# Optimization experiments

Hardware: AMD Instinct MI355X
Metric: run time of the kernel (lower is better)

Reference implementation:

```python
import jax, jax.numpy as jnp
import numpy as np
import math

NUM_PARAM = 9
STRIDE = 1
BN_EPS = 1e-5


def _make_p_n(N):
    # matches LDConv._get_p_n: irregular kernel offset grid of N points
    base = round(math.sqrt(N))
    rows = N // base
    mod = N % base
    gx, gy = np.meshgrid(np.arange(rows), np.arange(base), indexing='ij')
    px, py = gx.ravel(), gy.ravel()
    if mod > 0:
        mx, my = np.meshgrid(np.arange(rows, rows + 1), np.arange(mod), indexing='ij')
        px = np.concatenate([px, mx.ravel()])
        py = np.concatenate([py, my.ravel()])
    return jnp.asarray(np.concatenate([px, py]), jnp.float32).reshape(1, 2 * N, 1, 1)


def _conv2d_same(x, w, stride, pad):
    return jax.lax.conv_general_dilated(
        x, w, (stride, stride), [(pad, pad), (pad, pad)],
        dimension_numbers=('NCHW', 'OIHW', 'NCHW'))


def _gather(xf, q, W, N):
    # xf: (b,c,H*W); q: (b,h,w,2N) int indices -> (b,c,h,w,N)
    idx = q[..., :N] * W + q[..., N:]
    return jax.vmap(lambda xb, ib: xb[:, ib])(xf, idx)


def setup_inputs() -> dict:
    key = jax.random.key(0)
    ks = jax.random.split(key, 3)
    B, C, H, W = 8, 128, 64, 64
    outc = 256
    x = jax.random.normal(ks[0], (B, C, H, W), jnp.float32)
    # p_conv init: uniform(-1e-4, 1e-4) weights, zero bias (per the torch module)
    p_conv_w = jax.random.uniform(ks[1], (2 * NUM_PARAM, C, 3, 3), jnp.float32, -1e-4, 1e-4)
    p_conv_b = jnp.zeros((2 * NUM_PARAM,), jnp.float32)
    conv_w = jax.random.normal(ks[2], (outc, C, NUM_PARAM, 1), jnp.float32) / math.sqrt(C * NUM_PARAM)
    bn_gamma = jnp.ones((outc,), jnp.float32)
    bn_beta = jnp.zeros((outc,), jnp.float32)
    bn_mean = jnp.zeros((outc,), jnp.float32)
    bn_var = jnp.ones((outc,), jnp.float32)
    return dict(x=x, p_conv_w=p_conv_w, p_conv_b=p_conv_b, conv_w=conv_w,
                bn_gamma=bn_gamma, bn_beta=bn_beta, bn_mean=bn_mean, bn_var=bn_var)


def reference(x, p_conv_w, p_conv_b, conv_w, bn_gamma, bn_beta, bn_mean, bn_var):
    N = NUM_PARAM
    B, C, H, W = x.shape
    offset = _conv2d_same(x, p_conv_w, STRIDE, 1) + p_conv_b[None, :, None, None]  # (b,2N,h,w)
    h, w = offset.shape[2], offset.shape[3]
    gx, gy = jnp.meshgrid(jnp.arange(0, h * STRIDE, STRIDE),
                          jnp.arange(0, w * STRIDE, STRIDE), indexing='ij')
    p_0 = jnp.concatenate([jnp.broadcast_to(gx, (1, N, h, w)),
                           jnp.broadcast_to(gy, (1, N, h, w))], axis=1).astype(x.dtype)
    p = (p_0 + _make_p_n(N) + offset).transpose(0, 2, 3, 1)  # (b,h,w,2N)

    q_lt = jnp.floor(jax.lax.stop_gradient(p))
    q_rb = q_lt + 1
    clampi = lambda q: jnp.concatenate([jnp.clip(q[..., :N], 0, H - 1),
                                        jnp.clip(q[..., N:], 0, W - 1)], -1).astype(jnp.int32)
    q_lt = clampi(q_lt)
    q_rb = clampi(q_rb)
    q_lb = jnp.concatenate([q_lt[..., :N], q_rb[..., N:]], -1)
    q_rt = jnp.concatenate([q_rb[..., :N], q_lt[..., N:]], -1)
    p = jnp.concatenate([jnp.clip(p[..., :N], 0, H - 1),
                         jnp.clip(p[..., N:], 0, W - 1)], -1)
    f = lambda q: q.astype(p.dtype)
    g_lt = (1 + (f(q_lt[..., :N]) - p[..., :N])) * (1 + (f(q_lt[..., N:]) - p[..., N:]))
    g_rb = (1 - (f(q_rb[..., :N]) - p[..., :N])) * (1 - (f(q_rb[..., N:]) - p[..., N:]))
    g_lb = (1 + (f(q_lb[..., :N]) - p[..., :N])) * (1 - (f(q_lb[..., N:]) - p[..., N:]))
    g_rt = (1 - (f(q_rt[..., :N]) - p[..., :N])) * (1 + (f(q_rt[..., N:]) - p[..., N:]))

    xf = x.reshape(B, C, H * W)
    x_off = (g_lt[:, None] * _gather(xf, q_lt, W, N)
             + g_rb[:, None] * _gather(xf, q_rb, W, N)
             + g_lb[:, None] * _gather(xf, q_lb, W, N)
             + g_rt[:, None] * _gather(xf, q_rt, W, N))  # (b,c,h,w,N)
    # rearrange 'b c h w n -> b c (h n) w'
    x_off = x_off.transpose(0, 1, 2, 4, 3).reshape(B, C, h * N, w)

    y = jax.lax.conv_general_dilated(x_off, conv_w, (N, 1), 'VALID',
                                     dimension_numbers=('NCHW', 'OIHW', 'NCHW'))
    scale = (bn_gamma / jnp.sqrt(bn_var + BN_EPS))[None, :, None, None]
    y = (y - bn_mean[None, :, None, None]) * scale + bn_beta[None, :, None, None]
    return y * jax.nn.sigmoid(y)  # SiLU
```

## Files before the change

### kernel.cpp

```cpp
#include <hip/hip_runtime.h>
#include <hip/hip_bf16.h>
#include <cstdint>

#define B_   8
#define C_   128
#define H_   64
#define W_   64
#define NPT  9
#define OC   256
#define K_   (C_*NPT)
#define HW   (H_*W_)

typedef __attribute__((ext_vector_type(8))) short short8;
typedef __attribute__((ext_vector_type(4))) float f32x4;
typedef __attribute__((ext_vector_type(4))) unsigned int u32x4;

static __device__ __forceinline__ unsigned short f2bf(float f) {
    union { float f; unsigned u; } a; a.f = f;
    unsigned r = a.u + 0x7fffu + ((a.u >> 16) & 1u);
    return (unsigned short)(r >> 16);
}
static __device__ __forceinline__ float bf2f(unsigned short u) {
    union { unsigned u; float f; } a; a.u = ((unsigned)u) << 16;
    return a.f;
}

__global__ __launch_bounds__(512) void k_offset3(const float* __restrict__ x,
                                                 const float* __restrict__ wT,
                                                 const float* __restrict__ pb,
                                                 float* __restrict__ off) {
    __shared__ float red[8 * 64 * 19];
    int bid = blockIdx.x;
    int wg = (bid & 7) * 32 + (bid >> 3);
    int b = wg >> 5;
    int i0 = (wg & 31) * 2;
    int t = threadIdx.x;
    int j = t & 63;
    int cg = t >> 6;
    int cgu = __builtin_amdgcn_readfirstlane(cg);

    const float* xb = x + (size_t)b * C_ * HW;
    float acc[2][18];
#pragma unroll
    for (int p = 0; p < 2; ++p)
#pragma unroll
        for (int o = 0; o < 18; ++o) acc[p][o] = 0.f;

    for (int cc = 0; cc < 16; ++cc) {
        int c = cgu * 16 + cc;
        const float* xc = xb + (size_t)c * HW;
        float xv[4][3];
#pragma unroll
        for (int q = 0; q < 4; ++q) {
            int row = i0 - 1 + q;
            if (row >= 0 && row < H_) {
                const float* xr = xc + row * W_;
                xv[q][1] = xr[j];
                xv[q][0] = (j > 0)  ? xr[j - 1] : 0.f;
                xv[q][2] = (j < 63) ? xr[j + 1] : 0.f;
            } else {
                xv[q][0] = xv[q][1] = xv[q][2] = 0.f;
            }
        }
        const float* wp = wT + (size_t)c * 9 * 18;
#pragma unroll
        for (int tap = 0; tap < 9; ++tap) {
            const int kh = tap / 3, kw = tap % 3;
            float w18[18];
            *(f32x4*)(w18 + 0)  = *(const f32x4*)(wp + tap * 18 + 0);
            *(f32x4*)(w18 + 4)  = *(const f32x4*)(wp + tap * 18 + 4);
            *(f32x4*)(w18 + 8)  = *(const f32x4*)(wp + tap * 18 + 8);
            *(f32x4*)(w18 + 12) = *(const f32x4*)(wp + tap * 18 + 12);
            w18[16] = wp[tap * 18 + 16];
            w18[17] = wp[tap * 18 + 17];
#pragma unroll
            for (int p = 0; p < 2; ++p) {
                float xval = xv[p + kh][kw];
#pragma unroll
                for (int o = 0; o < 18; ++o) acc[p][o] += w18[o] * xval;
            }
        }
    }

#pragma unroll
    for (int p = 0; p < 2; ++p) {
        __syncthreads();
#pragma unroll
        for (int o = 0; o < 18; ++o) red[(cg * 64 + j) * 19 + o] = acc[p][o];
        __syncthreads();
        for (int e = t; e < 64 * 18; e += 512) {
            int jj = e / 18, o = e - jj * 18;
            float s = 0.f;
#pragma unroll
            for (int g = 0; g < 8; ++g) s += red[(g * 64 + jj) * 19 + o];
            off[(((size_t)b * 18 + o) * H_ + (i0 + p)) * W_ + jj] = s + pb[o];
        }
    }
}

__global__ __launch_bounds__(256) void k_prepwt(const float* __restrict__ pw,
                                                float* __restrict__ wT) {
    int idx = blockIdx.x * 256 + threadIdx.x;
    int ct = idx / 18;
    int o = idx - ct * 18;
    wT[idx] = pw[o * K_ + ct];
}

__global__ __launch_bounds__(256) void k_prepw(const float* __restrict__ cw,
                                               const float* __restrict__ gam,
                                               const float* __restrict__ bet,
                                               const float* __restrict__ mu,
                                               const float* __restrict__ var,
                                               __hip_bfloat16* __restrict__ wbf,
                                               float* __restrict__ bias) {
    int idx = blockIdx.x * 256 + threadIdx.x;
    int oc = idx / K_;
    int r = idx - oc * K_;
    int n = r >> 7;
    int c = r & 127;
    float sc = gam[oc] * rsqrtf(var[oc] + 1e-5f);
    wbf[idx] = __float2bfloat16(cw[oc * K_ + c * NPT + n] * sc);
    if (blockIdx.x == 0 && threadIdx.x < OC) {
        int o = threadIdx.x;
        float s = gam[o] * rsqrtf(var[o] + 1e-5f);
        bias[o] = bet[o] - mu[o] * s;
    }
}

__global__ __launch_bounds__(512) void k_fused(const float* __restrict__ x,
                                               const float* __restrict__ off,
                                               const __hip_bfloat16* __restrict__ wbf,
                                               const float* __restrict__ bias,
                                               float* __restrict__ out) {
    __shared__ __align__(16) char smem[81920];
    int bid = blockIdx.x;
    int wg = (bid & 7) * 64 + (bid >> 3);
    int b = wg >> 6;
    int i = wg & 63;
    int tid = threadIdx.x;
    int wv = tid >> 6, lane = tid & 63;
    int j = lane;
    int lrow = lane & 15, lg = lane >> 4;

    const float* xb = x + (size_t)b * C_ * HW;
#pragma unroll 4
    for (int it = 0; it < 20; ++it) {
        int ch = it * 512 + tid;
        int c4 = ch & 15;
        int c  = (ch >> 4) & 127;
        int s  = ch >> 11;
        int gr = min(63, max(0, i - 1 + s));
        f32x4 v = *(const f32x4*)(xb + (size_t)c * HW + gr * 64 + c4 * 4);
        int g = c >> 3;
        int sub = (c & 7) * 2;
#pragma unroll
        for (int k2 = 0; k2 < 4; ++k2) {
            int col = c4 * 4 + k2;
            *(unsigned short*)(smem + (s * 64 + col) * 256 + (((g ^ (col & 15)) << 4) + sub)) = f2bf(v[k2]);
        }
    }
    __syncthreads();

    const float* offb = off + (size_t)b * 18 * HW + i * 64 + j;
    u32x4 a_reg[18];
#pragma unroll
    for (int kt = 0; kt < 18; ++kt) {
        int idx = kt * 8 + wv;
        int n = idx >> 4;
        int c8 = idx & 15;
        float ox = offb[(size_t)n * HW];
        float oy = offb[(size_t)(n + 9) * HW];
        float pxf = (float)(i + n / 3) + ox;
        float pyf = (float)(j + n % 3) + oy;
        float fx = floorf(pxf), fy = floorf(pyf);
        int r0 = max(0, min(63, (int)fx));
        int r1 = max(0, min(63, (int)fx + 1));
        int c0 = max(0, min(63, (int)fy));
        int c1 = max(0, min(63, (int)fy + 1));
        float pxc = fminf(fmaxf(pxf, 0.f), 63.f);
        float pyc = fminf(fmaxf(pyf, 0.f), 63.f);
        float ax = 1.f + ((float)r0 - pxc);
        float bx = 1.f - ((float)r1 - pxc);
        float ay = 1.f + ((float)c0 - pyc);
        float by = 1.f - ((float)c1 - pyc);
        float w00 = ax * ay, w11 = bx * by, w01 = ax * by, w10 = bx * ay;
        int s0 = max(0, min(4, r0 - (i - 1)));
        int s1 = max(0, min(4, r1 - (i - 1)));
        short8 t00 = *(const short8*)(smem + (s0 * 64 + c0) * 256 + ((c8 ^ (c0 & 15)) << 4));
        short8 t11 = *(const short8*)(smem + (s1 * 64 + c1) * 256 + ((c8 ^ (c1 & 15)) << 4));
        short8 t01 = *(const short8*)(smem + (s0 * 64 + c1) * 256 + ((c8 ^ (c1 & 15)) << 4));
        short8 t10 = *(const short8*)(smem + (s1 * 64 + c0) * 256 + ((c8 ^ (c0 & 15)) << 4));
        u32x4 pk;
#pragma unroll
        for (int p2 = 0; p2 < 4; ++p2) {
            unsigned short rr[2];
#pragma unroll
            for (int e = 0; e < 2; ++e) {
                int ei = p2 * 2 + e;
                float v = w00 * bf2f((unsigned short)t00[ei])
                        + w11 * bf2f((unsigned short)t11[ei])
                        + w01 * bf2f((unsigned short)t01[ei])
                        + w10 * bf2f((unsigned short)t10[ei]);
                rr[e] = f2bf(v);
            }
            pk[p2] = (uint32_t)rr[0] | ((uint32_t)rr[1] << 16);
        }
        a_reg[kt] = pk;
    }
    __syncthreads();

    const char* Bb = (const char*)wbf;
    auto stage = [&](int buf, int kt, const u32x4& ag) {
        char* bbase = smem + 16384 + buf * 32768;
#pragma unroll
        for (int q = 0; q < 4; ++q) {
            int ch = q * 512 + tid;
            int row = ch >> 3, slot = ch & 7;
            int srcoff = row * (K_ * 2) + kt * 128 + ((slot * 16) ^ ((row & 7) << 4));
            __builtin_amdgcn_global_load_lds(
                (const __attribute__((address_space(1))) uint32_t*)(Bb + srcoff),
                (__attribute__((address_space(3))) uint32_t*)(bbase + ch * 16), 16, 0, 0);
        }
        *(u32x4*)(smem + buf * 8192 + wv * 1024 + lane * 16) = ag;
    };

    f32x4 zero = {0.f, 0.f, 0.f, 0.f};
    f32x4 acc[4][2];
#pragma unroll
    for (int m = 0; m < 4; ++m)
#pragma unroll
        for (int n = 0; n < 2; ++n) acc[m][n] = zero;

    stage(0, 0, a_reg[0]);
#pragma unroll
    for (int kt = 0; kt < 18; ++kt) {
        if (kt + 1 < 18) stage((kt + 1) & 1, kt + 1, a_reg[kt + 1]);
        __syncthreads();
        const char* sa = smem + (kt & 1) * 8192;
        const char* sb = smem + 16384 + (kt & 1) * 32768;
#pragma unroll
        for (int kk = 0; kk < 2; ++kk) {
            short8 afr[4], bfr[2];
#pragma unroll
            for (int m = 0; m < 4; ++m)
                afr[m] = *(const short8*)(sa + (kk * 4 + lg) * 1024 + (m * 16 + lrow) * 16);
#pragma unroll
            for (int n = 0; n < 2; ++n) {
                int row = wv * 32 + n * 16 + lrow;
                bfr[n] = *(const short8*)(sb + row * 128 + ((kk * 64 + lg * 16) ^ ((row & 7) << 4)));
            }
#pragma unroll
            for (int m = 0; m < 4; ++m)
#pragma unroll
                for (int n = 0; n < 2; ++n)
                    acc[m][n] = __builtin_amdgcn_mfma_f32_16x16x32_bf16(afr[m], bfr[n], acc[m][n], 0, 0, 0);
        }
        __syncthreads();
    }

#pragma unroll
    for (int n = 0; n < 2; ++n) {
        int oc = wv * 32 + n * 16 + lrow;
        float bs = bias[oc];
#pragma unroll
        for (int m = 0; m < 4; ++m) {
#pragma unroll
            for (int r = 0; r < 4; ++r) {
                int px = m * 16 + lg * 4 + r;
                float v = acc[m][n][r] + bs;
                float sv = v / (1.f + __expf(-v));
                out[((size_t)b * OC + oc) * HW + i * 64 + px] = sv;
            }
        }
    }
}

extern "C" void kernel_launch(void* const* d_in, const int* in_sizes, int n_in,
                              void* d_out, int out_size, void* d_ws, size_t ws_size,
                              hipStream_t stream) {
    const float* x   = (const float*)d_in[0];
    const float* pw  = (const float*)d_in[1];
    const float* pb  = (const float*)d_in[2];
    const float* cw  = (const float*)d_in[3];
    const float* gam = (const float*)d_in[4];
    const float* bet = (const float*)d_in[5];
    const float* mu  = (const float*)d_in[6];
    const float* var = (const float*)d_in[7];
    float* out = (float*)d_out;

    char* ws = (char*)d_ws;
    float* off           = (float*)ws;
    __hip_bfloat16* wbf  = (__hip_bfloat16*)(ws + 2359296);
    float* bias          = (float*)(ws + 2949120);
    float* wT            = (float*)(ws + 2950144);

    hipLaunchKernelGGL(k_prepwt,  dim3(81),   dim3(256), 0, stream, pw, wT);
    hipLaunchKernelGGL(k_offset3, dim3(256),  dim3(512), 0, stream, x, wT, pb, off);
    hipLaunchKernelGGL(k_prepw,   dim3(1152), dim3(256), 0, stream, cw, gam, bet, mu, var, wbf, bias);
    hipLaunchKernelGGL(k_fused,   dim3(512),  dim3(512), 0, stream, x, off, wbf, bias, out);
}
```

Before: 114.8 us.

## Gather bilinear samples from global channel-last bf16 copy, pipeline weight loads with gather

Adds a transpose kernel that writes x as channel-last bf16, so the fused kernel gathers bilinear corners directly from global memory instead of first staging five rows in LDS. The fused kernel now interleaves gathering for the next K-tile with MFMA on the current one, using half-tile weight staging with triple buffering, and keeps per-row offsets in LDS. The offset conv kernel is changed to one output row per block with 512 blocks. The cost is an extra kernel launch, an extra pass over x, and gather loads that can now miss cache.

```diff
diff --git a/kernel.cpp b/kernel.cpp
--- a/kernel.cpp
+++ b/kernel.cpp
@@ -25,36 +25,43 @@
     return a.f;
 }
 
-__global__ __launch_bounds__(512) void k_offset3(const float* __restrict__ x,
+__global__ __launch_bounds__(256) void k_prepwt(const float* __restrict__ pw,
+                                                float* __restrict__ wT) {
+    int idx = blockIdx.x * 256 + threadIdx.x;
+    int ct = idx / 18;
+    int o = idx - ct * 18;
+    wT[idx] = pw[o * K_ + ct];
+}
+
+__global__ __launch_bounds__(512) void k_offset4(const float* __restrict__ x,
                                                  const float* __restrict__ wT,
                                                  const float* __restrict__ pb,
                                                  float* __restrict__ off) {
     __shared__ float red[8 * 64 * 19];
     int bid = blockIdx.x;
-    int wg = (bid & 7) * 32 + (bid >> 3);
-    int b = wg >> 5;
-    int i0 = (wg & 31) * 2;
+    int wg = (bid & 7) * 64 + (bid >> 3);
+    int b = wg >> 6;
+    int i = wg & 63;
     int t = threadIdx.x;
     int j = t & 63;
     int cg = t >> 6;
     int cgu = __builtin_amdgcn_readfirstlane(cg);
 
+    float acc[18];
+#pragma unroll
+    for (int o = 0; o < 18; ++o) acc[o] = 0.f;
+
     const float* xb = x + (size_t)b * C_ * HW;
-    float acc[2][18];
-#pragma unroll
-    for (int p = 0; p < 2; ++p)
-#pragma unroll
-        for (int o = 0; o < 18; ++o) acc[p][o] = 0.f;
-
+#pragma unroll 2
     for (int cc = 0; cc < 16; ++cc) {
         int c = cgu * 16 + cc;
-        const float* xc = xb + (size_t)c * HW;
-        float xv[4][3];
-#pragma unroll
-        for (int q = 0; q < 4; ++q) {
-            int row = i0 - 1 + q;
+        const float* xc = xb + (size_t)c * HW + i * 64;
+        float xv[3][3];
+#pragma unroll
+        for (int q = 0; q < 3; ++q) {
+            int row = i - 1 + q;
             if (row >= 0 && row < H_) {
-                const float* xr = xc + row * W_;
+                const float* xr = xc + (q - 1) * 64;
                 xv[q][1] = xr[j];
                 xv[q][0] = (j > 0)  ? xr[j - 1] : 0.f;
                 xv[q][2] = (j < 63) ? xr[j + 1] : 0.f;
@@ -62,48 +69,25 @@
                 xv[q][0] = xv[q][1] = xv[q][2] = 0.f;
             }
         }
-        const float* wp = wT + (size_t)c * 9 * 18;
+        const float* wp = wT + (size_t)c * 162;
 #pragma unroll
         for (int tap = 0; tap < 9; ++tap) {
-            const int kh = tap / 3, kw = tap % 3;
-            float w18[18];
-            *(f32x4*)(w18 + 0)  = *(const f32x4*)(wp + tap * 18 + 0);
-            *(f32x4*)(w18 + 4)  = *(const f32x4*)(wp + tap * 18 + 4);
-            *(f32x4*)(w18 + 8)  = *(const f32x4*)(wp + tap * 18 + 8);
-            *(f32x4*)(w18 + 12) = *(const f32x4*)(wp + tap * 18 + 12);
-            w18[16] = wp[tap * 18 + 16];
-            w18[17] = wp[tap * 18 + 17];
-#pragma unroll
-            for (int p = 0; p < 2; ++p) {
-                float xval = xv[p + kh][kw];
-#pragma unroll
-                for (int o = 0; o < 18; ++o) acc[p][o] += w18[o] * xval;
-            }
-        }
-    }
-
-#pragma unroll
-    for (int p = 0; p < 2; ++p) {
-        __syncthreads();
-#pragma unroll
-        for (int o = 0; o < 18; ++o) red[(cg * 64 + j) * 19 + o] = acc[p][o];
-        __syncthreads();
-        for (int e = t; e < 64 * 18; e += 512) {
-            int jj = e / 18, o = e - jj * 18;
-            float s = 0.f;
-#pragma unroll
-            for (int g = 0; g < 8; ++g) s += red[(g * 64 + jj) * 19 + o];
-            off[(((size_t)b * 18 + o) * H_ + (i0 + p)) * W_ + jj] = s + pb[o];
-        }
-    }
-}
-
-__global__ __launch_bounds__(256) void k_prepwt(const float* __restrict__ pw,
-                                                float* __restrict__ wT) {
-    int idx = blockIdx.x * 256 + threadIdx.x;
-    int ct = idx / 18;
-    int o = idx - ct * 18;
-    wT[idx] = pw[o * K_ + ct];
+            float xval = xv[tap / 3][tap % 3];
+#pragma unroll
+            for (int o = 0; o < 18; ++o) acc[o] += wp[tap * 18 + o] * xval;
+        }
+    }
+
+#pragma unroll
+    for (int o = 0; o < 18; ++o) red[(cg * 64 + j) * 19 + o] = acc[o];
+    __syncthreads();
+    for (int e = t; e < 64 * 18; e += 512) {
+        int jj = e / 18, o = e - jj * 18;
+        float s = 0.f;
+#pragma unroll
+        for (int g = 0; g < 8; ++g) s += red[(g * 64 + jj) * 19 + o];
+        off[(((size_t)b * 18 + o) * H_ + i) * W_ + jj] = s + pb[o];
+    }
 }
 
 __global__ __launch_bounds__(256) void k_prepw(const float* __restrict__ cw,
@@ -111,7 +95,7 @@
                                                const float* __restrict__ bet,
                                                const float* __restrict__ mu,
                                                const float* __restrict__ var,
-                                               __hip_bfloat16* __restrict__ wbf,
+                                               unsigned short* __restrict__ wbf,
                                                float* __restrict__ bias) {
     int idx = blockIdx.x * 256 + threadIdx.x;
     int oc = idx / K_;
@@ -119,7 +103,7 @@
     int n = r >> 7;
     int c = r & 127;
     float sc = gam[oc] * rsqrtf(var[oc] + 1e-5f);
-    wbf[idx] = __float2bfloat16(cw[oc * K_ + c * NPT + n] * sc);
+    wbf[idx] = f2bf(cw[oc * K_ + c * NPT + n] * sc);
     if (blockIdx.x == 0 && threadIdx.x < OC) {
         int o = threadIdx.x;
         float s = gam[o] * rsqrtf(var[o] + 1e-5f);
@@ -127,49 +111,72 @@
     }
 }
 
-__global__ __launch_bounds__(512) void k_fused(const float* __restrict__ x,
-                                               const float* __restrict__ off,
-                                               const __hip_bfloat16* __restrict__ wbf,
-                                               const float* __restrict__ bias,
-                                               float* __restrict__ out) {
-    __shared__ __align__(16) char smem[81920];
+__global__ __launch_bounds__(256) void k_transpose(const float* __restrict__ x,
+                                                   unsigned short* __restrict__ xT) {
+    __shared__ float sp[128][65];
+    int b = blockIdx.x >> 6, i = blockIdx.x & 63;
+    int t = threadIdx.x;
+    const float* xb = x + (size_t)b * C_ * HW + i * 64;
+#pragma unroll
+    for (int it = 0; it < 8; ++it) {
+        int q = it * 256 + t;
+        int c = q >> 4, j4 = q & 15;
+        f32x4 v = *(const f32x4*)(xb + (size_t)c * HW + j4 * 4);
+        *(f32x4*)&sp[c][j4 * 4] = v;
+    }
+    __syncthreads();
+    unsigned short* xo = xT + ((size_t)b * HW + i * 64) * C_;
+#pragma unroll
+    for (int it = 0; it < 4; ++it) {
+        int q = it * 256 + t;
+        int j = q >> 4, cg = q & 15;
+        u32x4 pk;
+#pragma unroll
+        for (int p2 = 0; p2 < 4; ++p2) {
+            pk[p2] = (uint32_t)f2bf(sp[cg * 8 + p2 * 2][j])
+                   | ((uint32_t)f2bf(sp[cg * 8 + p2 * 2 + 1][j]) << 16);
+        }
+        *(u32x4*)(xo + (size_t)j * C_ + cg * 8) = pk;
+    }
+}
+
+__global__ __launch_bounds__(512, 4) void k_fused(const unsigned short* __restrict__ xT,
+                                                  const float* __restrict__ off,
+                                                  const unsigned short* __restrict__ wbf,
+                                                  const float* __restrict__ bias,
+                                                  float* __restrict__ out) {
+    __shared__ __align__(16) char smem[70144];
     int bid = blockIdx.x;
     int wg = (bid & 7) * 64 + (bid >> 3);
     int b = wg >> 6;
     int i = wg & 63;
     int tid = threadIdx.x;
-    int wv = tid >> 6, lane = tid & 63;
-    int j = lane;
+    int wv = tid >> 6, lane = tid & 63, j = lane;
     int lrow = lane & 15, lg = lane >> 4;
-
-    const float* xb = x + (size_t)b * C_ * HW;
-#pragma unroll 4
-    for (int it = 0; it < 20; ++it) {
-        int ch = it * 512 + tid;
-        int c4 = ch & 15;
-        int c  = (ch >> 4) & 127;
-        int s  = ch >> 11;
-        int gr = min(63, max(0, i - 1 + s));
-        f32x4 v = *(const f32x4*)(xb + (size_t)c * HW + gr * 64 + c4 * 4);
-        int g = c >> 3;
-        int sub = (c & 7) * 2;
-#pragma unroll
-        for (int k2 = 0; k2 < 4; ++k2) {
-            int col = c4 * 4 + k2;
-            *(unsigned short*)(smem + (s * 64 + col) * 256 + (((g ^ (col & 15)) << 4) + sub)) = f2bf(v[k2]);
-        }
-    }
-    __syncthreads();
-
-    const float* offb = off + (size_t)b * 18 * HW + i * 64 + j;
-    u32x4 a_reg[18];
-#pragma unroll
-    for (int kt = 0; kt < 18; ++kt) {
-        int idx = kt * 8 + wv;
-        int n = idx >> 4;
-        int c8 = idx & 15;
-        float ox = offb[(size_t)n * HW];
-        float oy = offb[(size_t)(n + 9) * HW];
+    const unsigned short* xTb = xT + (size_t)b * HW * C_;
+    const char* Bb = (const char*)wbf;
+    float* soff = (float*)(smem + 65536);
+
+    auto stageB = [&](int buf, int hs) {
+        char* base = smem + 16384 + buf * 16384;
+#pragma unroll
+        for (int q = 0; q < 2; ++q) {
+            int ch = q * 512 + tid;
+            int row = ch >> 2, slot = ch & 3;
+            int src = row * 2304 + hs * 64 + slot * 16;
+            __builtin_amdgcn_global_load_lds(
+                (const __attribute__((address_space(1))) uint32_t*)(Bb + src),
+                (__attribute__((address_space(3))) uint32_t*)(base + ch * 16), 16, 0, 0);
+        }
+    };
+
+    short8 tp0, tp1, tp2, tp3;
+    float w00, w11, w01, w10;
+    auto gather_issue = [&](int kt) {
+        int n = kt >> 1;
+        int c8 = (kt & 1) * 8 + wv;
+        float ox = soff[n * 64 + j];
+        float oy = soff[(n + 9) * 64 + j];
         float pxf = (float)(i + n / 3) + ox;
         float pyf = (float)(j + n % 3) + oy;
         float fx = floorf(pxf), fy = floorf(pyf);
@@ -183,13 +190,14 @@
         float bx = 1.f - ((float)r1 - pxc);
         float ay = 1.f + ((float)c0 - pyc);
         float by = 1.f - ((float)c1 - pyc);
-        float w00 = ax * ay, w11 = bx * by, w01 = ax * by, w10 = bx * ay;
-        int s0 = max(0, min(4, r0 - (i - 1)));
-        int s1 = max(0, min(4, r1 - (i - 1)));
-        short8 t00 = *(const short8*)(smem + (s0 * 64 + c0) * 256 + ((c8 ^ (c0 & 15)) << 4));
-        short8 t11 = *(const short8*)(smem + (s1 * 64 + c1) * 256 + ((c8 ^ (c1 & 15)) << 4));
-        short8 t01 = *(const short8*)(smem + (s0 * 64 + c1) * 256 + ((c8 ^ (c1 & 15)) << 4));
-        short8 t10 = *(const short8*)(smem + (s1 * 64 + c0) * 256 + ((c8 ^ (c0 & 15)) << 4));
+        w00 = ax * ay; w11 = bx * by; w01 = ax * by; w10 = bx * ay;
+        const unsigned short* g = xTb + c8 * 8;
+        tp0 = *(const short8*)(g + (size_t)(r0 * 64 + c0) * C_);
+        tp1 = *(const short8*)(g + (size_t)(r1 * 64 + c1) * C_);
+        tp2 = *(const short8*)(g + (size_t)(r0 * 64 + c1) * C_);
+        tp3 = *(const short8*)(g + (size_t)(r1 * 64 + c0) * C_);
+    };
+    auto bilinear_write = [&](int kt) {
         u32x4 pk;
 #pragma unroll
         for (int p2 = 0; p2 < 4; ++p2) {
@@ -197,31 +205,15 @@
 #pragma unroll
             for (int e = 0; e < 2; ++e) {
                 int ei = p2 * 2 + e;
-                float v = w00 * bf2f((unsigned short)t00[ei])
-                        + w11 * bf2f((unsigned short)t11[ei])
-                        + w01 * bf2f((unsigned short)t01[ei])
-                        + w10 * bf2f((unsigned short)t10[ei]);
+                float v = w00 * bf2f((unsigned short)tp0[ei])
+                        + w11 * bf2f((unsigned short)tp1[ei])
+                        + w01 * bf2f((unsigned short)tp2[ei])
+                        + w10 * bf2f((unsigned short)tp3[ei]);
                 rr[e] = f2bf(v);
             }
             pk[p2] = (uint32_t)rr[0] | ((uint32_t)rr[1] << 16);
         }
-        a_reg[kt] = pk;
-    }
-    __syncthreads();
-
-    const char* Bb = (const char*)wbf;
-    auto stage = [&](int buf, int kt, const u32x4& ag) {
-        char* bbase = smem + 16384 + buf * 32768;
-#pragma unroll
-        for (int q = 0; q < 4; ++q) {
-            int ch = q * 512 + tid;
-            int row = ch >> 3, slot = ch & 7;
-            int srcoff = row * (K_ * 2) + kt * 128 + ((slot * 16) ^ ((row & 7) << 4));
-            __builtin_amdgcn_global_load_lds(
-                (const __attribute__((address_space(1))) uint32_t*)(Bb + srcoff),
-                (__attribute__((address_space(3))) uint32_t*)(bbase + ch * 16), 16, 0, 0);
-        }
-        *(u32x4*)(smem + buf * 8192 + wv * 1024 + lane * 16) = ag;
+        *(u32x4*)(smem + (kt & 1) * 8192 + wv * 1024 + j * 16) = pk;
     };
 
     f32x4 zero = {0.f, 0.f, 0.f, 0.f};
@@ -231,30 +223,47 @@
 #pragma unroll
         for (int n = 0; n < 2; ++n) acc[m][n] = zero;
 
-    stage(0, 0, a_reg[0]);
-#pragma unroll
+    auto compute_half = [&](int abuf, int bbuf, int h) {
+        const char* sa = smem + abuf * 8192;
+        const char* sb = smem + 16384 + bbuf * 16384;
+        short8 afr[4], bfr[2];
+#pragma unroll
+        for (int m = 0; m < 4; ++m)
+            afr[m] = *(const short8*)(sa + (h * 4 + lg) * 1024 + (m * 16 + lrow) * 16);
+#pragma unroll
+        for (int n = 0; n < 2; ++n) {
+            int row = wv * 32 + n * 16 + lrow;
+            bfr[n] = *(const short8*)(sb + row * 64 + lg * 16);
+        }
+#pragma unroll
+        for (int m = 0; m < 4; ++m)
+#pragma unroll
+            for (int n = 0; n < 2; ++n)
+                acc[m][n] = __builtin_amdgcn_mfma_f32_16x16x32_bf16(afr[m], bfr[n], acc[m][n], 0, 0, 0);
+    };
+
+    for (int e = tid; e < 1152; e += 512) {
+        int plane = e >> 6, jj = e & 63;
+        soff[e] = off[(((size_t)b * 18 + plane) * H_ + i) * W_ + jj];
+    }
+    stageB(0, 0);
+    stageB(1, 1);
+    __syncthreads();
+    gather_issue(0);
+    bilinear_write(0);
+    stageB(2, 2);
+    __syncthreads();
+
+#pragma unroll 6
     for (int kt = 0; kt < 18; ++kt) {
-        if (kt + 1 < 18) stage((kt + 1) & 1, kt + 1, a_reg[kt + 1]);
+        const int hs0 = 2 * kt;
+        if (hs0 + 2 < 36) stageB((hs0 + 2) % 3, hs0 + 2);
+        if (kt < 17) gather_issue(kt + 1);
+        compute_half(kt & 1, hs0 % 3, 0);
         __syncthreads();
-        const char* sa = smem + (kt & 1) * 8192;
-        const char* sb = smem + 16384 + (kt & 1) * 32768;
-#pragma unroll
-        for (int kk = 0; kk < 2; ++kk) {
-            short8 afr[4], bfr[2];
-#pragma unroll
-            for (int m = 0; m < 4; ++m)
-                afr[m] = *(const short8*)(sa + (kk * 4 + lg) * 1024 + (m * 16 + lrow) * 16);
-#pragma unroll
-            for (int n = 0; n < 2; ++n) {
-                int row = wv * 32 + n * 16 + lrow;
-                bfr[n] = *(const short8*)(sb + row * 128 + ((kk * 64 + lg * 16) ^ ((row & 7) << 4)));
-            }
-#pragma unroll
-            for (int m = 0; m < 4; ++m)
-#pragma unroll
-                for (int n = 0; n < 2; ++n)
-                    acc[m][n] = __builtin_amdgcn_mfma_f32_16x16x32_bf16(afr[m], bfr[n], acc[m][n], 0, 0, 0);
-        }
+        if (hs0 + 3 < 36) stageB((hs0 + 3) % 3, hs0 + 3);
+        if (kt < 17) bilinear_write(kt + 1);
+        compute_half(kt & 1, (hs0 + 1) % 3, 1);
         __syncthreads();
     }
 
@@ -290,12 +299,14 @@
 
     char* ws = (char*)d_ws;
     float* off           = (float*)ws;
-    __hip_bfloat16* wbf  = (__hip_bfloat16*)(ws + 2359296);
+    unsigned short* wbf  = (unsigned short*)(ws + 2359296);
     float* bias          = (float*)(ws + 2949120);
     float* wT            = (float*)(ws + 2950144);
-
-    hipLaunchKernelGGL(k_prepwt,  dim3(81),   dim3(256), 0, stream, pw, wT);
-    hipLaunchKernelGGL(k_offset3, dim3(256),  dim3(512), 0, stream, x, wT, pb, off);
-    hipLaunchKernelGGL(k_prepw,   dim3(1152), dim3(256), 0, stream, cw, gam, bet, mu, var, wbf, bias);
-    hipLaunchKernelGGL(k_fused,   dim3(512),  dim3(512), 0, stream, x, off, wbf, bias, out);
-}
+    unsigned short* xT   = (unsigned short*)(ws + 3033088);
+
+    hipLaunchKernelGGL(k_prepwt,    dim3(81),   dim3(256), 0, stream, pw, wT);
+    hipLaunchKernelGGL(k_prepw,     dim3(1152), dim3(256), 0, stream, cw, gam, bet, mu, var, wbf, bias);
+    hipLaunchKernelGGL(k_transpose, dim3(512),  dim3(256), 0, stream, x, xT);
+    hipLaunchKernelGGL(k_offset4,   dim3(512),  dim3(512), 0, stream, x, wT, pb, off);
+    hipLaunchKernelGGL(k_fused,     dim3(512),  dim3(512), 0, stream, xT, off, wbf, bias, out);
+}
```

Result: slower. 150.7 us (+31.3%).
